# Performance work log

Hardware: AMD Instinct MI355X
Metric: run time of the kernel (lower is better)

## Reference

```python
import jax, jax.numpy as jnp
import numpy as np

B, F, M, C = 4096, 2048, 14, 100
K = 2 ** M  # 16384 latent binary codes


def _codebook(m):
    # itertools.product([0,1], repeat=m) order: row i is binary repr of i, MSB first
    i = jnp.arange(2 ** m)
    j = jnp.arange(m)
    return ((i[:, None] >> (m - 1 - j)[None, :]) & 1).astype(jnp.float32)  # [K, m]


def setup_inputs() -> dict:
    key = jax.random.key(0)
    k1, k2, k3, k4, k5, k6 = jax.random.split(key, 6)
    init_a = 2.0 / np.sqrt(F)
    init_b = 2.0 / np.sqrt(M)
    return {
        "x_in": jax.random.normal(k1, (B, F), dtype=jnp.float32),
        "y_in": jax.random.randint(k2, (B,), 0, C),
        "alpha_0": jax.random.normal(k3, (M,), dtype=jnp.float32),
        "alpha": init_a * jax.random.normal(k4, (M, F), dtype=jnp.float32),
        "beta_0": jax.random.normal(k5, (C,), dtype=jnp.float32),
        "beta": init_b * jax.random.normal(k6, (C, M), dtype=jnp.float32),
    }


def reference(x_in, y_in, alpha_0, alpha, beta_0, beta):
    cb = _codebook(M)  # [K, M]
    # linear_eta
    le = alpha_0[None, :] + x_in @ alpha.T  # [B, M]
    # linear_pi over all codes (mod_codes = 2*cb - 1)
    linear_pi = beta_0[:, None] + beta @ (2.0 * cb - 1.0).T  # [C, K]
    pi = jax.nn.softmax(linear_pi, axis=0)  # exp / sum over classes
    # P(Z|X): exp(cb @ le.T - sum_j softplus(le)) transposed -> [B, K]
    sp = jax.nn.softplus(le)  # log(1 + exp(le)), stable  [B, M]
    P_ZgivenX = jnp.exp((cb @ le.T - jnp.sum(sp, axis=1)[None, :]).T)  # [B, K]
    y1 = jax.nn.one_hot(y_in, C, dtype=le.dtype)  # [B, C]
    numerator = (y1 @ pi) * P_ZgivenX  # [B, K]
    denom = jnp.sum(numerator, axis=1)  # [B]
    # E[Ind Z_j]: masked sum over codes with bit j == 1 == single matmul with cb
    E_IndZ = (numerator @ cb) / denom[:, None]  # [B, M]
    # EI
    EZ = 2.0 * E_IndZ - 1.0
    EI = jnp.sum(y1 * (beta_0[None, :] + EZ @ beta.T))
    # EII
    prob_log = numerator / denom[:, None]
    log_terms = jax.scipy.special.logsumexp(linear_pi, axis=0)  # [K]
    EII = jnp.sum(prob_log * log_terms[None, :])
    # EIII, EIV
    EIII = jnp.sum(E_IndZ * le)
    EIV = jnp.sum(sp)
    return EI - EII + EIII - EIV
```

## Files before the change

kernel.cpp:

```cpp
#include <hip/hip_runtime.h>
#include <math.h>

#define NB 4096
#define NF 2048
#define NM 14
#define NC 100
#define NK 16384

__device__ __forceinline__ float softplus_f(float v) {
    return fmaxf(v, 0.f) + log1pf(__expf(-fabsf(v)));
}

extern "C" __global__ void __launch_bounds__(256) kA(
        const float* __restrict__ x, const float* __restrict__ alpha,
        float* __restrict__ le_part,
        const float* __restrict__ beta, const float* __restrict__ beta0,
        float2* __restrict__ SL, unsigned int* __restrict__ cnt) {
    const int tid = threadIdx.x;
    if (blockIdx.x < 512) {
        const int wave = tid >> 6, lane = tid & 63;
        const int grp = (int)blockIdx.x >> 1;
        const int half = blockIdx.x & 1;
        const int row0 = grp * 16 + wave * 4;
        const float4* __restrict__ x4 = (const float4*)x;
        const float4* __restrict__ a4 = (const float4*)alpha;
        float acc[4][NM];
#pragma unroll
        for (int r = 0; r < 4; ++r)
#pragma unroll
            for (int j = 0; j < NM; ++j) acc[r][j] = 0.f;
#pragma unroll 1
        for (int cc = 0; cc < 4; ++cc) {
            const int f4i = half * 256 + cc * 64 + lane;
            float4 av[NM];
#pragma unroll
            for (int j = 0; j < NM; ++j) av[j] = a4[j * 512 + f4i];
#pragma unroll
            for (int r = 0; r < 4; ++r) {
                const float4 xv = x4[(row0 + r) * 512 + f4i];
#pragma unroll
                for (int j = 0; j < NM; ++j) {
                    acc[r][j] = fmaf(xv.x, av[j].x, acc[r][j]);
                    acc[r][j] = fmaf(xv.y, av[j].y, acc[r][j]);
                    acc[r][j] = fmaf(xv.z, av[j].z, acc[r][j]);
                    acc[r][j] = fmaf(xv.w, av[j].w, acc[r][j]);
                }
            }
        }
#pragma unroll
        for (int m = 1; m < 64; m <<= 1) {
#pragma unroll
            for (int r = 0; r < 4; ++r)
#pragma unroll
                for (int j = 0; j < NM; ++j)
                    acc[r][j] += __shfl_xor(acc[r][j], m, 64);
        }
        if (lane == 0) {
            float* dst = le_part + half * (NB * NM) + row0 * NM;
#pragma unroll
            for (int r = 0; r < 4; ++r)
#pragma unroll
                for (int j = 0; j < NM; ++j)
                    dst[r * NM + j] = acc[r][j];
        }
    } else {
        __shared__ float b2[NC * NM];
        __shared__ float base_s[NC];
        __shared__ float Sp[4][64];
        const int kb = (int)blockIdx.x - 512;
        if (kb == 0 && tid == 0) *cnt = 0u;
        for (int i = tid; i < NC * NM; i += 256) b2[i] = 2.f * beta[i];
        if (tid < NC) {
            float s = beta0[tid];
            for (int j = 0; j < NM; ++j) s -= beta[tid * NM + j];
            base_s[tid] = s;
        }
        __syncthreads();
        const int kl = tid & 63, q = tid >> 6;
        const int k = kb * 64 + kl;
        float bits[NM];
#pragma unroll
        for (int j = 0; j < NM; ++j) bits[j] = (float)((k >> (13 - j)) & 1);
        float S = 0.f;
        for (int c = q * 25; c < q * 25 + 25; ++c) {
            float d = base_s[c];
#pragma unroll
            for (int j = 0; j < NM; ++j) d = fmaf(bits[j], b2[c * NM + j], d);
            S += __expf(d);
        }
        Sp[q][kl] = S;
        __syncthreads();
        if (tid < 64) {
            const float Sf = Sp[0][tid] + Sp[1][tid] + Sp[2][tid] + Sp[3][tid];
            SL[kb * 64 + tid] = make_float2(1.f / Sf, __logf(Sf));
        }
    }
}

extern "C" __global__ void __launch_bounds__(256) k3_main(
        const float* __restrict__ le_part, const float* __restrict__ alpha0,
        const int* __restrict__ y, const float* __restrict__ beta,
        const float* __restrict__ beta0, const float2* __restrict__ SL,
        float* __restrict__ partial, unsigned int* __restrict__ cnt,
        float* __restrict__ out) {
    __shared__ float t_s[8][16];
    __shared__ float sp_s[8][16];
    __shared__ float cs_s[8];
    __shared__ float f_s[8];
    __shared__ float EAlds[128][8];
    __shared__ float Elds[128][8];
    __shared__ float red[4][16];
    __shared__ unsigned last_s;
    const int tid = threadIdx.x;
    const int b0 = blockIdx.x * 8;

    if (tid < 128) {
        const int r = tid >> 4, j = tid & 15;
        if (j < NM) {
            const int yv = y[b0 + r];
            const float lv = le_part[(b0 + r) * NM + j]
                           + le_part[NB * NM + (b0 + r) * NM + j] + alpha0[j];
            t_s[r][j] = lv + 2.f * beta[yv * NM + j];
            sp_s[r][j] = softplus_f(lv);
        }
    }
    __syncthreads();
    if (tid < 8) {
        const int yv = y[b0 + tid];
        float cs = beta0[yv];
        for (int j = 0; j < NM; ++j) {
            cs -= beta[yv * NM + j];
            cs += fmaxf(t_s[tid][j], 0.f) - sp_s[tid][j];
        }
        cs_s[tid] = cs;
    }
#pragma unroll
    for (int e = 0; e < 4; ++e) {
        const int idx = tid + 256 * e;
        const int r = idx & 7, h = idx >> 3;
        float A = 0.f, ub = 0.f;
#pragma unroll
        for (int j = 0; j < 7; ++j) {
            const float tv = t_s[r][j];
            A += ((h >> (6 - j)) & 1) ? tv : 0.f;
            ub += fmaxf(tv, 0.f);
        }
        const float Ap = A - ub;
        const float E = __expf(Ap);
        Elds[h][r] = E;
        EAlds[h][r] = E * Ap;
    }
    const int l = tid & 127;
    float eb[8], aterm[8];
#pragma unroll
    for (int r = 0; r < 8; ++r) {
        float A = 0.f, ub = 0.f;
#pragma unroll
        for (int j = 7; j < NM; ++j) {
            const float tv = t_s[r][j];
            A += ((l >> (13 - j)) & 1) ? tv : 0.f;
            ub += fmaxf(tv, 0.f);
        }
        aterm[r] = A - ub;
        eb[r] = __expf(A - ub);
    }
    __syncthreads();

    float U[8], V[8];
#pragma unroll
    for (int r = 0; r < 8; ++r) { U[r] = 0.f; V[r] = 0.f; }
    const int c = tid >> 7;
#pragma unroll 4
    for (int i = 0; i < 64; ++i) {
        const float2 sl = SL[i * 256 + tid];
        const float xw = sl.x;
        const float zw = sl.x * sl.y;
        const int h = 2 * i + c;
        const float4 Pa = *(const float4*)&EAlds[h][0];
        const float4 Pb = *(const float4*)&EAlds[h][4];
        const float4 Ea = *(const float4*)&Elds[h][0];
        const float4 Eb = *(const float4*)&Elds[h][4];
        const float Pr[8] = {Pa.x, Pa.y, Pa.z, Pa.w, Pb.x, Pb.y, Pb.z, Pb.w};
        const float Er[8] = {Ea.x, Ea.y, Ea.z, Ea.w, Eb.x, Eb.y, Eb.z, Eb.w};
#pragma unroll
        for (int r = 0; r < 8; ++r) {
            U[r] = fmaf(Er[r], xw, U[r]);
            V[r] = fmaf(Pr[r], xw, V[r]);
            V[r] = fmaf(Er[r], -zw, V[r]);
        }
    }
    float vals[16];
#pragma unroll
    for (int r = 0; r < 8; ++r) {
        vals[r] = eb[r] * U[r];
        vals[8 + r] = eb[r] * fmaf(aterm[r], U[r], V[r]);
    }
#pragma unroll
    for (int m = 1; m < 64; m <<= 1)
#pragma unroll
        for (int q2 = 0; q2 < 16; ++q2)
            vals[q2] += __shfl_xor(vals[q2], m, 64);
    const int wv = tid >> 6, lane = tid & 63;
    if (lane == 0) {
#pragma unroll
        for (int q2 = 0; q2 < 16; ++q2) red[wv][q2] = vals[q2];
    }
    __syncthreads();
    if (tid < 16)
        red[0][tid] = red[0][tid] + red[1][tid] + red[2][tid] + red[3][tid];
    __syncthreads();
    if (tid < 8)
        f_s[tid] = cs_s[tid] + red[0][8 + tid] / red[0][tid];
    __syncthreads();
    if (tid == 0) {
        float s = 0.f;
#pragma unroll
        for (int r = 0; r < 8; ++r) s += f_s[r];
        __hip_atomic_store(&partial[blockIdx.x], s, __ATOMIC_RELEASE,
                           __HIP_MEMORY_SCOPE_AGENT);
        const unsigned old = __hip_atomic_fetch_add(cnt, 1u, __ATOMIC_ACQ_REL,
                                                    __HIP_MEMORY_SCOPE_AGENT);
        last_s = (old == 511u) ? 1u : 0u;
    }
    __syncthreads();
    if (last_s) {
        float s = __hip_atomic_load(&partial[tid], __ATOMIC_RELAXED,
                                    __HIP_MEMORY_SCOPE_AGENT)
                + __hip_atomic_load(&partial[tid + 256], __ATOMIC_RELAXED,
                                    __HIP_MEMORY_SCOPE_AGENT);
#pragma unroll
        for (int m = 1; m < 64; m <<= 1) s += __shfl_xor(s, m, 64);
        if (lane == 0) red[0][wv] = s;
        __syncthreads();
        if (tid == 0) out[0] = red[0][0] + red[0][1] + red[0][2] + red[0][3];
    }
}

extern "C" void kernel_launch(void* const* d_in, const int* in_sizes, int n_in,
                              void* d_out, int out_size, void* d_ws, size_t ws_size,
                              hipStream_t stream) {
    const float* x      = (const float*)d_in[0];
    const int*   y      = (const int*)d_in[1];
    const float* alpha0 = (const float*)d_in[2];
    const float* alpha  = (const float*)d_in[3];
    const float* beta0  = (const float*)d_in[4];
    const float* beta   = (const float*)d_in[5];

    char* ws = (char*)d_ws;
    float*        le_part = (float*)ws;
    float2*       SL      = (float2*)(ws + 2 * NB * NM * 4);
    float*        partial = (float*)(ws + 2 * NB * NM * 4 + NK * 8);
    unsigned int* cnt     = (unsigned int*)(ws + 2 * NB * NM * 4 + NK * 8 + 512 * 4);
    float*        out     = (float*)d_out;

    kA<<<768, 256, 0, stream>>>(x, alpha, le_part, beta, beta0, SL, cnt);
    k3_main<<<512, 256, 0, stream>>>(le_part, alpha0, y, beta, beta0, SL,
                                     partial, cnt, out);
}
```

Before: 117.0 us.

## Fuse x@alpha projection into main kernel and precompute log-sum-exp ratio

The x·alpha^T projection moves out of the first kernel into the main kernel, so each block computes its own 8 rows of le directly and the le_part workspace round trip through global memory goes away. The first kernel now only builds the per-code softmax normalizer and stores logS/S in place of logS, which removes one multiply per element in the main loop. Alpha is now re-read by all 512 blocks, where before 512 blocks each read half of it, and register pressure rises from holding 16 float4 x values per thread. A launch_bounds occupancy hint of 2 is added to offset this.

```diff
diff --git a/kernel.cpp b/kernel.cpp
--- a/kernel.cpp
+++ b/kernel.cpp
@@ -7,98 +7,51 @@
 #define NC 100
 #define NK 16384
 
+typedef float nf4 __attribute__((ext_vector_type(4)));
+
 __device__ __forceinline__ float softplus_f(float v) {
     return fmaxf(v, 0.f) + log1pf(__expf(-fabsf(v)));
 }
 
-extern "C" __global__ void __launch_bounds__(256) kA(
-        const float* __restrict__ x, const float* __restrict__ alpha,
-        float* __restrict__ le_part,
+extern "C" __global__ void __launch_bounds__(256) k2_sl(
         const float* __restrict__ beta, const float* __restrict__ beta0,
         float2* __restrict__ SL, unsigned int* __restrict__ cnt) {
+    __shared__ float b2[NC * NM];
+    __shared__ float base_s[NC];
+    __shared__ float Sp[4][64];
     const int tid = threadIdx.x;
-    if (blockIdx.x < 512) {
-        const int wave = tid >> 6, lane = tid & 63;
-        const int grp = (int)blockIdx.x >> 1;
-        const int half = blockIdx.x & 1;
-        const int row0 = grp * 16 + wave * 4;
-        const float4* __restrict__ x4 = (const float4*)x;
-        const float4* __restrict__ a4 = (const float4*)alpha;
-        float acc[4][NM];
-#pragma unroll
-        for (int r = 0; r < 4; ++r)
-#pragma unroll
-            for (int j = 0; j < NM; ++j) acc[r][j] = 0.f;
-#pragma unroll 1
-        for (int cc = 0; cc < 4; ++cc) {
-            const int f4i = half * 256 + cc * 64 + lane;
-            float4 av[NM];
-#pragma unroll
-            for (int j = 0; j < NM; ++j) av[j] = a4[j * 512 + f4i];
-#pragma unroll
-            for (int r = 0; r < 4; ++r) {
-                const float4 xv = x4[(row0 + r) * 512 + f4i];
-#pragma unroll
-                for (int j = 0; j < NM; ++j) {
-                    acc[r][j] = fmaf(xv.x, av[j].x, acc[r][j]);
-                    acc[r][j] = fmaf(xv.y, av[j].y, acc[r][j]);
-                    acc[r][j] = fmaf(xv.z, av[j].z, acc[r][j]);
-                    acc[r][j] = fmaf(xv.w, av[j].w, acc[r][j]);
-                }
-            }
-        }
-#pragma unroll
-        for (int m = 1; m < 64; m <<= 1) {
-#pragma unroll
-            for (int r = 0; r < 4; ++r)
-#pragma unroll
-                for (int j = 0; j < NM; ++j)
-                    acc[r][j] += __shfl_xor(acc[r][j], m, 64);
-        }
-        if (lane == 0) {
-            float* dst = le_part + half * (NB * NM) + row0 * NM;
-#pragma unroll
-            for (int r = 0; r < 4; ++r)
-#pragma unroll
-                for (int j = 0; j < NM; ++j)
-                    dst[r * NM + j] = acc[r][j];
-        }
-    } else {
-        __shared__ float b2[NC * NM];
-        __shared__ float base_s[NC];
-        __shared__ float Sp[4][64];
-        const int kb = (int)blockIdx.x - 512;
-        if (kb == 0 && tid == 0) *cnt = 0u;
-        for (int i = tid; i < NC * NM; i += 256) b2[i] = 2.f * beta[i];
-        if (tid < NC) {
-            float s = beta0[tid];
-            for (int j = 0; j < NM; ++j) s -= beta[tid * NM + j];
-            base_s[tid] = s;
-        }
-        __syncthreads();
-        const int kl = tid & 63, q = tid >> 6;
-        const int k = kb * 64 + kl;
-        float bits[NM];
-#pragma unroll
-        for (int j = 0; j < NM; ++j) bits[j] = (float)((k >> (13 - j)) & 1);
-        float S = 0.f;
-        for (int c = q * 25; c < q * 25 + 25; ++c) {
-            float d = base_s[c];
-#pragma unroll
-            for (int j = 0; j < NM; ++j) d = fmaf(bits[j], b2[c * NM + j], d);
-            S += __expf(d);
-        }
-        Sp[q][kl] = S;
-        __syncthreads();
-        if (tid < 64) {
-            const float Sf = Sp[0][tid] + Sp[1][tid] + Sp[2][tid] + Sp[3][tid];
-            SL[kb * 64 + tid] = make_float2(1.f / Sf, __logf(Sf));
-        }
-    }
-}
-
-extern "C" __global__ void __launch_bounds__(256) k3_main(
-        const float* __restrict__ le_part, const float* __restrict__ alpha0,
+    if (blockIdx.x == 0 && tid == 0) *cnt = 0u;
+    for (int i = tid; i < NC * NM; i += 256) b2[i] = 2.f * beta[i];
+    if (tid < NC) {
+        float s = beta0[tid];
+        for (int j = 0; j < NM; ++j) s -= beta[tid * NM + j];
+        base_s[tid] = s;
+    }
+    __syncthreads();
+    const int kl = tid & 63, q = tid >> 6;
+    const int k = blockIdx.x * 64 + kl;
+    float bits[NM];
+#pragma unroll
+    for (int j = 0; j < NM; ++j) bits[j] = (float)((k >> (13 - j)) & 1);
+    float S = 0.f;
+    for (int c = q * 25; c < q * 25 + 25; ++c) {
+        float d = base_s[c];
+#pragma unroll
+        for (int j = 0; j < NM; ++j) d = fmaf(bits[j], b2[c * NM + j], d);
+        S += __expf(d);
+    }
+    Sp[q][kl] = S;
+    __syncthreads();
+    if (tid < 64) {
+        const float Sf = Sp[0][tid] + Sp[1][tid] + Sp[2][tid] + Sp[3][tid];
+        const float inv = 1.f / Sf;
+        SL[blockIdx.x * 64 + tid] = make_float2(inv, __logf(Sf) * inv);
+    }
+}
+
+extern "C" __global__ void __launch_bounds__(256, 2) k3_main(
+        const float* __restrict__ x, const float* __restrict__ alpha,
+        const float* __restrict__ alpha0,
         const int* __restrict__ y, const float* __restrict__ beta,
         const float* __restrict__ beta0, const float2* __restrict__ SL,
         float* __restrict__ partial, unsigned int* __restrict__ cnt,
@@ -114,17 +67,47 @@
     const int tid = threadIdx.x;
     const int b0 = blockIdx.x * 8;
 
-    if (tid < 128) {
-        const int r = tid >> 4, j = tid & 15;
-        if (j < NM) {
-            const int yv = y[b0 + r];
-            const float lv = le_part[(b0 + r) * NM + j]
-                           + le_part[NB * NM + (b0 + r) * NM + j] + alpha0[j];
-            t_s[r][j] = lv + 2.f * beta[yv * NM + j];
-            sp_s[r][j] = softplus_f(lv);
-        }
-    }
-    __syncthreads();
+    {
+        const int rw = tid >> 5, fl = tid & 31;
+        const nf4* __restrict__ x4 = (const nf4*)x;
+        const float4* __restrict__ a4 = (const float4*)alpha;
+        const int rowbase = (b0 + rw) * 512;
+        nf4 xv[16];
+#pragma unroll
+        for (int cc = 0; cc < 16; ++cc)
+            xv[cc] = __builtin_nontemporal_load(&x4[rowbase + cc * 32 + fl]);
+        float acc[NM];
+#pragma unroll
+        for (int j = 0; j < NM; ++j) acc[j] = 0.f;
+#pragma unroll
+        for (int cc = 0; cc < 16; ++cc) {
+            const nf4 xc = xv[cc];
+#pragma unroll
+            for (int j = 0; j < NM; ++j) {
+                const float4 av = a4[j * 512 + cc * 32 + fl];
+                acc[j] = fmaf(xc.x, av.x, acc[j]);
+                acc[j] = fmaf(xc.y, av.y, acc[j]);
+                acc[j] = fmaf(xc.z, av.z, acc[j]);
+                acc[j] = fmaf(xc.w, av.w, acc[j]);
+            }
+        }
+#pragma unroll
+        for (int m = 1; m < 32; m <<= 1)
+#pragma unroll
+            for (int j = 0; j < NM; ++j)
+                acc[j] += __shfl_xor(acc[j], m, 64);
+        if (fl == 0) {
+            const int yv = y[b0 + rw];
+#pragma unroll
+            for (int j = 0; j < NM; ++j) {
+                const float lv = acc[j] + alpha0[j];
+                t_s[rw][j] = lv + 2.f * beta[yv * NM + j];
+                sp_s[rw][j] = softplus_f(lv);
+            }
+        }
+    }
+    __syncthreads();
+
     if (tid < 8) {
         const int yv = y[b0 + tid];
         float cs = beta0[yv];
@@ -174,7 +157,7 @@
     for (int i = 0; i < 64; ++i) {
         const float2 sl = SL[i * 256 + tid];
         const float xw = sl.x;
-        const float zw = sl.x * sl.y;
+        const float zw = sl.y;
         const int h = 2 * i + c;
         const float4 Pa = *(const float4*)&EAlds[h][0];
         const float4 Pb = *(const float4*)&EAlds[h][4];
@@ -247,13 +230,12 @@
     const float* beta   = (const float*)d_in[5];
 
     char* ws = (char*)d_ws;
-    float*        le_part = (float*)ws;
-    float2*       SL      = (float2*)(ws + 2 * NB * NM * 4);
-    float*        partial = (float*)(ws + 2 * NB * NM * 4 + NK * 8);
-    unsigned int* cnt     = (unsigned int*)(ws + 2 * NB * NM * 4 + NK * 8 + 512 * 4);
+    float2*       SL      = (float2*)ws;
+    float*        partial = (float*)(ws + NK * 8);
+    unsigned int* cnt     = (unsigned int*)(ws + NK * 8 + 512 * 4);
     float*        out     = (float*)d_out;
 
-    kA<<<768, 256, 0, stream>>>(x, alpha, le_part, beta, beta0, SL, cnt);
-    k3_main<<<512, 256, 0, stream>>>(le_part, alpha0, y, beta, beta0, SL,
+    k2_sl<<<256, 256, 0, stream>>>(beta, beta0, SL, cnt);
+    k3_main<<<512, 256, 0, stream>>>(x, alpha, alpha0, y, beta, beta0, SL,
                                      partial, cnt, out);
 }
```

New measurement: 128.0 us. 1.09x slower.

## Split feature dim into quarters and halve rows per block in main kernel

Applied to the files above, without the earlier changes.

The x@alpha.T partial-sum kernel now splits F into four chunks instead of two, producing 1024 blocks, and the main kernel processes 4 batch rows per block instead of 8, doubling its grid to 1024 blocks. Launch bounds now request a minimum of 3 and 4 blocks per CU. SL stores log(S)/S premultiplied so the inner loop drops one multiply. The aim is more parallelism and occupancy on the many-CU GPU. The cost is that each block re-reads the full SL table for fewer rows, doubling SL traffic, and the final reduction has more partials.

```diff
diff --git a/kernel.cpp b/kernel.cpp
--- a/kernel.cpp
+++ b/kernel.cpp
@@ -11,16 +11,16 @@
     return fmaxf(v, 0.f) + log1pf(__expf(-fabsf(v)));
 }
 
-extern "C" __global__ void __launch_bounds__(256) kA(
+extern "C" __global__ void __launch_bounds__(256, 3) kA(
         const float* __restrict__ x, const float* __restrict__ alpha,
         float* __restrict__ le_part,
         const float* __restrict__ beta, const float* __restrict__ beta0,
         float2* __restrict__ SL, unsigned int* __restrict__ cnt) {
     const int tid = threadIdx.x;
-    if (blockIdx.x < 512) {
+    if (blockIdx.x < 1024) {
         const int wave = tid >> 6, lane = tid & 63;
-        const int grp = (int)blockIdx.x >> 1;
-        const int half = blockIdx.x & 1;
+        const int grp = (int)blockIdx.x >> 2;
+        const int quarter = blockIdx.x & 3;
         const int row0 = grp * 16 + wave * 4;
         const float4* __restrict__ x4 = (const float4*)x;
         const float4* __restrict__ a4 = (const float4*)alpha;
@@ -30,8 +30,8 @@
 #pragma unroll
             for (int j = 0; j < NM; ++j) acc[r][j] = 0.f;
 #pragma unroll 1
-        for (int cc = 0; cc < 4; ++cc) {
-            const int f4i = half * 256 + cc * 64 + lane;
+        for (int cc = 0; cc < 2; ++cc) {
+            const int f4i = quarter * 128 + cc * 64 + lane;
             float4 av[NM];
 #pragma unroll
             for (int j = 0; j < NM; ++j) av[j] = a4[j * 512 + f4i];
@@ -56,7 +56,7 @@
                     acc[r][j] += __shfl_xor(acc[r][j], m, 64);
         }
         if (lane == 0) {
-            float* dst = le_part + half * (NB * NM) + row0 * NM;
+            float* dst = le_part + quarter * (NB * NM) + row0 * NM;
 #pragma unroll
             for (int r = 0; r < 4; ++r)
 #pragma unroll
@@ -67,7 +67,7 @@
         __shared__ float b2[NC * NM];
         __shared__ float base_s[NC];
         __shared__ float Sp[4][64];
-        const int kb = (int)blockIdx.x - 512;
+        const int kb = (int)blockIdx.x - 1024;
         if (kb == 0 && tid == 0) *cnt = 0u;
         for (int i = tid; i < NC * NM; i += 256) b2[i] = 2.f * beta[i];
         if (tid < NC) {
@@ -92,40 +92,44 @@
         __syncthreads();
         if (tid < 64) {
             const float Sf = Sp[0][tid] + Sp[1][tid] + Sp[2][tid] + Sp[3][tid];
-            SL[kb * 64 + tid] = make_float2(1.f / Sf, __logf(Sf));
-        }
-    }
-}
-
-extern "C" __global__ void __launch_bounds__(256) k3_main(
+            const float inv = 1.f / Sf;
+            SL[kb * 64 + tid] = make_float2(inv, __logf(Sf) * inv);
+        }
+    }
+}
+
+extern "C" __global__ void __launch_bounds__(256, 4) k3_main(
         const float* __restrict__ le_part, const float* __restrict__ alpha0,
         const int* __restrict__ y, const float* __restrict__ beta,
         const float* __restrict__ beta0, const float2* __restrict__ SL,
         float* __restrict__ partial, unsigned int* __restrict__ cnt,
         float* __restrict__ out) {
-    __shared__ float t_s[8][16];
-    __shared__ float sp_s[8][16];
-    __shared__ float cs_s[8];
-    __shared__ float f_s[8];
-    __shared__ float EAlds[128][8];
-    __shared__ float Elds[128][8];
-    __shared__ float red[4][16];
+    __shared__ float t_s[4][16];
+    __shared__ float sp_s[4][16];
+    __shared__ float cs_s[4];
+    __shared__ float f_s[4];
+    __shared__ float EAlds[128][4];
+    __shared__ float Elds[128][4];
+    __shared__ float red[4][8];
     __shared__ unsigned last_s;
     const int tid = threadIdx.x;
-    const int b0 = blockIdx.x * 8;
-
-    if (tid < 128) {
+    const int b0 = blockIdx.x * 4;
+
+    if (tid < 64) {
         const int r = tid >> 4, j = tid & 15;
         if (j < NM) {
-            const int yv = y[b0 + r];
-            const float lv = le_part[(b0 + r) * NM + j]
-                           + le_part[NB * NM + (b0 + r) * NM + j] + alpha0[j];
+            const int row = b0 + r;
+            const int yv = y[row];
+            const float lv = ((le_part[row * NM + j]
+                             + le_part[NB * NM + row * NM + j])
+                             + le_part[2 * NB * NM + row * NM + j])
+                             + le_part[3 * NB * NM + row * NM + j] + alpha0[j];
             t_s[r][j] = lv + 2.f * beta[yv * NM + j];
             sp_s[r][j] = softplus_f(lv);
         }
     }
     __syncthreads();
-    if (tid < 8) {
+    if (tid < 4) {
         const int yv = y[b0 + tid];
         float cs = beta0[yv];
         for (int j = 0; j < NM; ++j) {
@@ -135,9 +139,9 @@
         cs_s[tid] = cs;
     }
 #pragma unroll
-    for (int e = 0; e < 4; ++e) {
+    for (int e = 0; e < 2; ++e) {
         const int idx = tid + 256 * e;
-        const int r = idx & 7, h = idx >> 3;
+        const int r = idx & 3, h = idx >> 2;
         float A = 0.f, ub = 0.f;
 #pragma unroll
         for (int j = 0; j < 7; ++j) {
@@ -151,9 +155,9 @@
         EAlds[h][r] = E * Ap;
     }
     const int l = tid & 127;
-    float eb[8], aterm[8];
-#pragma unroll
-    for (int r = 0; r < 8; ++r) {
+    float eb[4], aterm[4];
+#pragma unroll
+    for (int r = 0; r < 4; ++r) {
         float A = 0.f, ub = 0.f;
 #pragma unroll
         for (int j = 7; j < NM; ++j) {
@@ -166,68 +170,70 @@
     }
     __syncthreads();
 
-    float U[8], V[8];
-#pragma unroll
-    for (int r = 0; r < 8; ++r) { U[r] = 0.f; V[r] = 0.f; }
+    float U[4], V[4];
+#pragma unroll
+    for (int r = 0; r < 4; ++r) { U[r] = 0.f; V[r] = 0.f; }
     const int c = tid >> 7;
 #pragma unroll 4
     for (int i = 0; i < 64; ++i) {
         const float2 sl = SL[i * 256 + tid];
         const float xw = sl.x;
-        const float zw = sl.x * sl.y;
+        const float zw = sl.y;
         const int h = 2 * i + c;
         const float4 Pa = *(const float4*)&EAlds[h][0];
-        const float4 Pb = *(const float4*)&EAlds[h][4];
         const float4 Ea = *(const float4*)&Elds[h][0];
-        const float4 Eb = *(const float4*)&Elds[h][4];
-        const float Pr[8] = {Pa.x, Pa.y, Pa.z, Pa.w, Pb.x, Pb.y, Pb.z, Pb.w};
-        const float Er[8] = {Ea.x, Ea.y, Ea.z, Ea.w, Eb.x, Eb.y, Eb.z, Eb.w};
-#pragma unroll
-        for (int r = 0; r < 8; ++r) {
+        const float Pr[4] = {Pa.x, Pa.y, Pa.z, Pa.w};
+        const float Er[4] = {Ea.x, Ea.y, Ea.z, Ea.w};
+#pragma unroll
+        for (int r = 0; r < 4; ++r) {
             U[r] = fmaf(Er[r], xw, U[r]);
             V[r] = fmaf(Pr[r], xw, V[r]);
             V[r] = fmaf(Er[r], -zw, V[r]);
         }
     }
-    float vals[16];
-#pragma unroll
-    for (int r = 0; r < 8; ++r) {
+    float vals[8];
+#pragma unroll
+    for (int r = 0; r < 4; ++r) {
         vals[r] = eb[r] * U[r];
-        vals[8 + r] = eb[r] * fmaf(aterm[r], U[r], V[r]);
+        vals[4 + r] = eb[r] * fmaf(aterm[r], U[r], V[r]);
     }
 #pragma unroll
     for (int m = 1; m < 64; m <<= 1)
 #pragma unroll
-        for (int q2 = 0; q2 < 16; ++q2)
+        for (int q2 = 0; q2 < 8; ++q2)
             vals[q2] += __shfl_xor(vals[q2], m, 64);
     const int wv = tid >> 6, lane = tid & 63;
     if (lane == 0) {
 #pragma unroll
-        for (int q2 = 0; q2 < 16; ++q2) red[wv][q2] = vals[q2];
-    }
-    __syncthreads();
-    if (tid < 16)
+        for (int q2 = 0; q2 < 8; ++q2) red[wv][q2] = vals[q2];
+    }
+    __syncthreads();
+    if (tid < 8)
         red[0][tid] = red[0][tid] + red[1][tid] + red[2][tid] + red[3][tid];
     __syncthreads();
-    if (tid < 8)
-        f_s[tid] = cs_s[tid] + red[0][8 + tid] / red[0][tid];
+    if (tid < 4)
+        f_s[tid] = cs_s[tid] + red[0][4 + tid] / red[0][tid];
     __syncthreads();
     if (tid == 0) {
         float s = 0.f;
 #pragma unroll
-        for (int r = 0; r < 8; ++r) s += f_s[r];
+        for (int r = 0; r < 4; ++r) s += f_s[r];
         __hip_atomic_store(&partial[blockIdx.x], s, __ATOMIC_RELEASE,
                            __HIP_MEMORY_SCOPE_AGENT);
         const unsigned old = __hip_atomic_fetch_add(cnt, 1u, __ATOMIC_ACQ_REL,
                                                     __HIP_MEMORY_SCOPE_AGENT);
-        last_s = (old == 511u) ? 1u : 0u;
+        last_s = (old == 1023u) ? 1u : 0u;
     }
     __syncthreads();
     if (last_s) {
-        float s = __hip_atomic_load(&partial[tid], __ATOMIC_RELAXED,
-                                    __HIP_MEMORY_SCOPE_AGENT)
-                + __hip_atomic_load(&partial[tid + 256], __ATOMIC_RELAXED,
-                                    __HIP_MEMORY_SCOPE_AGENT);
+        float s = (__hip_atomic_load(&partial[tid], __ATOMIC_RELAXED,
+                                     __HIP_MEMORY_SCOPE_AGENT)
+                 + __hip_atomic_load(&partial[tid + 256], __ATOMIC_RELAXED,
+                                     __HIP_MEMORY_SCOPE_AGENT))
+                + (__hip_atomic_load(&partial[tid + 512], __ATOMIC_RELAXED,
+                                     __HIP_MEMORY_SCOPE_AGENT)
+                 + __hip_atomic_load(&partial[tid + 768], __ATOMIC_RELAXED,
+                                     __HIP_MEMORY_SCOPE_AGENT));
 #pragma unroll
         for (int m = 1; m < 64; m <<= 1) s += __shfl_xor(s, m, 64);
         if (lane == 0) red[0][wv] = s;
@@ -248,12 +254,12 @@
 
     char* ws = (char*)d_ws;
     float*        le_part = (float*)ws;
-    float2*       SL      = (float2*)(ws + 2 * NB * NM * 4);
-    float*        partial = (float*)(ws + 2 * NB * NM * 4 + NK * 8);
-    unsigned int* cnt     = (unsigned int*)(ws + 2 * NB * NM * 4 + NK * 8 + 512 * 4);
+    float2*       SL      = (float2*)(ws + 4 * NB * NM * 4);
+    float*        partial = (float*)(ws + 4 * NB * NM * 4 + NK * 8);
+    unsigned int* cnt     = (unsigned int*)(ws + 4 * NB * NM * 4 + NK * 8 + 1024 * 4);
     float*        out     = (float*)d_out;
 
-    kA<<<768, 256, 0, stream>>>(x, alpha, le_part, beta, beta0, SL, cnt);
-    k3_main<<<512, 256, 0, stream>>>(le_part, alpha0, y, beta, beta0, SL,
-                                     partial, cnt, out);
-}
+    kA<<<1280, 256, 0, stream>>>(x, alpha, le_part, beta, beta0, SL, cnt);
+    k3_main<<<1024, 256, 0, stream>>>(le_part, alpha0, y, beta, beta0, SL,
+                                      partial, cnt, out);
+}
```

Result: slower. 139.8 us (+19.5%).
